# Optimization experiments

Measured on AMD Instinct MI355X. Metric: run time of the kernel, lower is better.

## Reference

```python
import jax, jax.numpy as jnp
import numpy as np

IN_FEATURES = 4096
OUT_FEATURES = 4096
GROUP_SIZE = 128


def _unpack_int4_last_dim(packed):
    # packed: [..., P] int32 -> [..., P*8] int32 nibbles in [0,15]
    shifts = jnp.arange(0, 32, 4, dtype=jnp.int32)
    u = (packed[..., None] >> shifts) & 15
    return u.reshape(*packed.shape[:-1], packed.shape[-1] * 8)


def setup_inputs() -> dict:
    key = jax.random.key(0)
    k1, k2, k3, k4, k5 = jax.random.split(key, 5)
    groups = IN_FEATURES // GROUP_SIZE  # 32
    x = jax.random.normal(k1, (4096, IN_FEATURES), dtype=jnp.float32)
    qweight = jax.random.randint(k2, (OUT_FEATURES, IN_FEATURES // 8), 0, 2147483647, dtype=jnp.int32)
    qzeros = jax.random.randint(k3, (OUT_FEATURES, groups // 8), 0, 2147483647, dtype=jnp.int32)
    scales = jax.random.uniform(k4, (OUT_FEATURES, groups), dtype=jnp.float32) * 0.02 + 0.001
    bias = jax.random.normal(k5, (OUT_FEATURES,), dtype=jnp.float32)
    return {"x": x, "qweight": qweight, "qzeros": qzeros, "scales": scales, "bias": bias}


def _dequantize_weight(qweight, qzeros, scales):
    # qweight: [out, in/8] -> w_int: [out, in]
    w_int = _unpack_int4_last_dim(qweight).astype(jnp.float32)
    # qzeros: [out, groups/8] -> zeros: [out, groups]
    zeros = _unpack_int4_last_dim(qzeros).astype(jnp.float32)
    group_ids = jnp.arange(IN_FEATURES) // GROUP_SIZE  # [in]
    # expand per-group scale/zero along in_features
    w = (w_int - zeros[:, group_ids]) * scales[:, group_ids]  # [out, in]
    return w


def reference(x, qweight, qzeros, scales, bias):
    w = _dequantize_weight(qweight, qzeros, scales)  # [out, in] fp32
    return x @ w.T + bias  # [tokens, out]
```

## Files before the change

### kernel.cpp

```cpp
#include <hip/hip_runtime.h>
#include <hip/hip_bf16.h>

#define TOKENS 4096
#define IN_F   4096
#define OUT_F  4096

typedef __bf16 bf16x8 __attribute__((ext_vector_type(8)));
typedef float  f32x4  __attribute__((ext_vector_type(4)));
typedef unsigned int u32;
typedef u32 u32x4 __attribute__((ext_vector_type(4)));

#define DEQ_BLOCKS 2048
#define CVT_BLOCKS 4096

__device__ __forceinline__ void gld_lds16(const void* g, void* l) {
    __builtin_amdgcn_global_load_lds(
        (const __attribute__((address_space(1))) u32*)g,
        (__attribute__((address_space(3))) u32*)l,
        16, 0, 0);
}

__global__ __launch_bounds__(256) void prep_kernel(
        const u32* __restrict__ qweight, const u32* __restrict__ qzeros,
        const float* __restrict__ scales, const float* __restrict__ x,
        __bf16* __restrict__ W, __bf16* __restrict__ A) {
    const int tid = threadIdx.x;
    if (blockIdx.x < DEQ_BLOCKS) {
        int idx4 = blockIdx.x * 256 + tid;
        int n  = idx4 >> 7;
        int p4 = (idx4 & 127) << 2;
        int g  = p4 >> 4;
        u32 qz = qzeros[(n << 2) + (g >> 3)];
        float z = (float)((qz >> ((g & 7) * 4)) & 15);
        float s = scales[(n << 5) + g];
        u32x4 qw = *(const u32x4*)(qweight + (size_t)n * 512 + p4);
        __bf16* dst = W + (size_t)n * IN_F + p4 * 8;
#pragma unroll
        for (int c = 0; c < 4; ++c) {
            bf16x8 h;
#pragma unroll
            for (int j = 0; j < 8; ++j) {
                float w = ((float)((qw[c] >> (4 * j)) & 15) - z) * s;
                h[j] = (__bf16)w;
            }
            *(bf16x8*)(dst + c * 8) = h;
        }
    } else {
        int idx = (blockIdx.x - DEQ_BLOCKS) * 256 + tid;
        const f32x4* xp = (const f32x4*)x + (size_t)idx * 4;
        f32x4 v0 = xp[0], v1 = xp[1], v2 = xp[2], v3 = xp[3];
        bf16x8 h0, h1;
#pragma unroll
        for (int j = 0; j < 4; ++j) {
            h0[j] = (__bf16)v0[j]; h0[4 + j] = (__bf16)v1[j];
            h1[j] = (__bf16)v2[j]; h1[4 + j] = (__bf16)v3[j];
        }
        bf16x8* ap = (bf16x8*)A + (size_t)idx * 2;
        ap[0] = h0; ap[1] = h1;
    }
}

__global__ __launch_bounds__(512, 2) void gemm8p(
        const __bf16* __restrict__ A, const __bf16* __restrict__ B,
        const float* __restrict__ bias, float* __restrict__ C) {
    __shared__ __align__(16) char lsA[65536];
    __shared__ __align__(16) char lsB[65536];

    const int t    = threadIdx.x;
    const int lane = t & 63, wave = t >> 6;
    const int lr   = lane & 15, quad = lane >> 4;
    const int wm   = (wave >> 2) * 128;
    const int wn   = (wave & 3) * 64;

    int bid = blockIdx.x;
    bid = (bid & 7) * 32 + (bid >> 3);
    const int bm = bid >> 4, bn = bid & 15;

    const __bf16* Abase = A + (size_t)bm * 256 * IN_F;
    const __bf16* Bbase = B + (size_t)bn * 256 * IN_F;

    const int srow0 = t >> 2;
    const int srow1 = 128 + (t >> 2);
    const int scol0 = ((t & 3) ^ ((srow0 >> 1) & 3)) * 8;
    const int scol1 = ((t & 3) ^ ((srow1 >> 1) & 3)) * 8;

#define STAGE(OPBASE, LS, KT, KH, BUF) do {                                  \
    int _kb = (((KT) & 63) * 64 + (KH) * 32);                                \
    gld_lds16(OPBASE + (size_t)srow0 * IN_F + _kb + scol0,                   \
              LS + ((BUF) * 2 + (KH)) * 16384 + t * 16);                     \
    gld_lds16(OPBASE + (size_t)srow1 * IN_F + _kb + scol1,                   \
              LS + ((BUF) * 2 + (KH)) * 16384 + 8192 + t * 16);              \
} while (0)

    const u32 slot16 = (u32)((quad ^ ((lr >> 1) & 3)) * 16);
    const u32 lsA0 = (u32)(size_t)(__attribute__((address_space(3))) char*)lsA;
    const u32 lsB0 = (u32)(size_t)(__attribute__((address_space(3))) char*)lsB;
    const u32 aA = lsA0 + (u32)((wm + lr) * 64) + slot16;
    const u32 aB = lsB0 + (u32)((wn + lr) * 64) + slot16;

    bf16x8 af[4], bfr[4];
    f32x4 acc[8][4] = {};

#define RA(BUF, KH) (((BUF) * 2 + (KH)) * 16384)
#define RB(BUF, KH) (((BUF) * 2 + (KH)) * 16384)

#define DSR(dst, base, OFF) do {                                             \
    u32x4 _r;                                                                \
    asm volatile("ds_read_b128 %0, %1 offset:%2"                             \
                 : "=v"(_r) : "v"(base), "n"(OFF));                          \
    dst = __builtin_bit_cast(bf16x8, _r);                                    \
} while (0)

#define MFMA4_I(PM, I) do {                                                  \
    _Pragma("unroll")                                                        \
    for (int j = 0; j < 4; ++j)                                              \
        acc[(PM) * 4 + (I)][j] = __builtin_amdgcn_mfma_f32_16x16x32_bf16(    \
            af[(I)], bfr[j], acc[(PM) * 4 + (I)][j], 0, 0, 0);               \
} while (0)

#define MFMA4_J(PM, J) do {                                                  \
    _Pragma("unroll")                                                        \
    for (int i = 0; i < 4; ++i)                                              \
        acc[(PM) * 4 + i][(J)] = __builtin_amdgcn_mfma_f32_16x16x32_bf16(    \
            af[i], bfr[(J)], acc[(PM) * 4 + i][(J)], 0, 0, 0);               \
} while (0)

#define FENCE() asm volatile("" ::: "memory")
#define BAR()  do { FENCE(); __builtin_amdgcn_s_barrier(); FENCE(); } while (0)
#define VM6()  asm volatile("s_waitcnt vmcnt(6)" ::: "memory")
#define VM4()  asm volatile("s_waitcnt vmcnt(4)" ::: "memory")
#define PRIO(x) __builtin_amdgcn_s_setprio(x)
#define SB()   __builtin_amdgcn_sched_barrier(0)
#define LGKM0SB() do {                                                       \
    asm volatile("s_waitcnt lgkmcnt(0)" ::: "memory"); SB(); } while (0)

#define P0_BODY(KT, B) do {                                                  \
    STAGE(Abase, lsA, (KT) + 1, 1, 1 - (B));                                 \
    LGKM0SB(); PRIO(1);                                                      \
    MFMA4_I(0,0); SB(); DSR(af[0], aA, RA(B,0)+4096+0*1024); SB();           \
    MFMA4_I(0,1); SB(); DSR(af[1], aA, RA(B,0)+4096+1*1024); SB();           \
    MFMA4_I(0,2); SB(); DSR(af[2], aA, RA(B,0)+4096+2*1024); SB();           \
    MFMA4_I(0,3); SB(); DSR(af[3], aA, RA(B,0)+4096+3*1024); SB();           \
    PRIO(0); BAR();                                                          \
} while (0)

#define P1_BODY(KT, B) do {                                                  \
    STAGE(Bbase, lsB, (KT) + 1, 1, 1 - (B));                                 \
    LGKM0SB(); PRIO(1);                                                      \
    MFMA4_J(1,0); SB(); DSR(bfr[0], aB, RB(B,1)+0*1024); SB();               \
    MFMA4_J(1,1); SB(); DSR(bfr[1], aB, RB(B,1)+1*1024); SB();               \
    MFMA4_J(1,2); SB(); DSR(bfr[2], aB, RB(B,1)+2*1024); SB();               \
    MFMA4_J(1,3); SB(); DSR(bfr[3], aB, RB(B,1)+3*1024); SB();               \
    DSR(af[0], aA, RA(B,1)+0*1024); DSR(af[1], aA, RA(B,1)+1*1024);          \
    DSR(af[2], aA, RA(B,1)+2*1024); DSR(af[3], aA, RA(B,1)+3*1024);          \
    PRIO(0); BAR();                                                          \
} while (0)

#define P2_BODY(KT, B) do {                                                  \
    STAGE(Abase, lsA, (KT) + 2, 0, (B));                                     \
    LGKM0SB(); PRIO(1);                                                      \
    MFMA4_I(0,0); SB(); DSR(af[0], aA, RA(B,1)+4096+0*1024); SB();           \
    MFMA4_I(0,1); SB(); DSR(af[1], aA, RA(B,1)+4096+1*1024); SB();           \
    MFMA4_I(0,2); SB(); DSR(af[2], aA, RA(B,1)+4096+2*1024); SB();           \
    MFMA4_I(0,3); SB(); DSR(af[3], aA, RA(B,1)+4096+3*1024); SB();           \
    PRIO(0); VM6(); BAR();                                                   \
} while (0)

#define P3_BODY(KT, B) do {                                                  \
    STAGE(Bbase, lsB, (KT) + 2, 0, (B));                                     \
    LGKM0SB(); PRIO(1);                                                      \
    MFMA4_J(1,0); SB(); DSR(bfr[0], aB, RB(1-(B),0)+0*1024); SB();           \
    MFMA4_J(1,1); SB(); DSR(bfr[1], aB, RB(1-(B),0)+1*1024); SB();           \
    MFMA4_J(1,2); SB(); DSR(bfr[2], aB, RB(1-(B),0)+2*1024); SB();           \
    MFMA4_J(1,3); SB(); DSR(bfr[3], aB, RB(1-(B),0)+3*1024); SB();           \
    DSR(af[0], aA, RA(1-(B),0)+0*1024); DSR(af[1], aA, RA(1-(B),0)+1*1024);  \
    DSR(af[2], aA, RA(1-(B),0)+2*1024); DSR(af[3], aA, RA(1-(B),0)+3*1024);  \
    PRIO(0); VM4(); BAR();                                                   \
} while (0)

    STAGE(Abase, lsA, 0, 0, 0);
    STAGE(Bbase, lsB, 0, 0, 0);
    STAGE(Abase, lsA, 0, 1, 0);
    STAGE(Bbase, lsB, 0, 1, 0);
    STAGE(Abase, lsA, 1, 0, 1);
    STAGE(Bbase, lsB, 1, 0, 1);
    VM4();
    BAR();
    DSR(bfr[0], aB, RB(0,0)+0*1024); DSR(bfr[1], aB, RB(0,0)+1*1024);
    DSR(bfr[2], aB, RB(0,0)+2*1024); DSR(bfr[3], aB, RB(0,0)+3*1024);
    DSR(af[0], aA, RA(0,0)+0*1024);  DSR(af[1], aA, RA(0,0)+1*1024);
    DSR(af[2], aA, RA(0,0)+2*1024);  DSR(af[3], aA, RA(0,0)+3*1024);

    for (int kt = 0; kt < 64; kt += 2) {
        P0_BODY(kt, 0); P1_BODY(kt, 0); P2_BODY(kt, 0); P3_BODY(kt, 0);
        P0_BODY(kt + 1, 1); P1_BODY(kt + 1, 1);
        P2_BODY(kt + 1, 1); P3_BODY(kt + 1, 1);
    }

    asm volatile("s_waitcnt vmcnt(0) lgkmcnt(0)" ::: "memory");

    const int row0 = bm * 256 + wm + quad * 4;
    const int col0 = bn * 256 + wn + lr;
#pragma unroll
    for (int j = 0; j < 4; ++j) {
        const int col = col0 + j * 16;
        const float bv = bias[col];
#pragma unroll
        for (int i = 0; i < 8; ++i) {
            const int row = row0 + i * 16;
#pragma unroll
            for (int r = 0; r < 4; ++r)
                C[(size_t)(row + r) * OUT_F + col] = acc[i][j][r] + bv;
        }
    }
}

extern "C" void kernel_launch(void* const* d_in, const int* in_sizes, int n_in,
                              void* d_out, int out_size, void* d_ws, size_t ws_size,
                              hipStream_t stream) {
    (void)in_sizes; (void)n_in; (void)out_size; (void)ws_size;
    const float* x       = (const float*)d_in[0];
    const u32*   qweight = (const u32*)d_in[1];
    const u32*   qzeros  = (const u32*)d_in[2];
    const float* scales  = (const float*)d_in[3];
    const float* bias    = (const float*)d_in[4];
    float* out = (float*)d_out;

    __bf16* W   = (__bf16*)d_ws;
    __bf16* Abf = (__bf16*)((char*)d_ws + (size_t)OUT_F * IN_F * 2);

    prep_kernel<<<dim3(DEQ_BLOCKS + CVT_BLOCKS), dim3(256), 0, stream>>>(
        qweight, qzeros, scales, x, W, Abf);
    gemm8p<<<dim3(256), dim3(512), 0, stream>>>(Abf, W, bias, out);
}
```

Measured before the change: 240.2 us.

## Double-buffer A/B fragment registers to overlap LDS reads with MFMA phases

```diff
diff --git a/kernel.cpp b/kernel.cpp
--- a/kernel.cpp
+++ b/kernel.cpp
@@ -98,7 +98,7 @@
     const u32 aA = lsA0 + (u32)((wm + lr) * 64) + slot16;
     const u32 aB = lsB0 + (u32)((wn + lr) * 64) + slot16;
 
-    bf16x8 af[4], bfr[4];
+    bf16x8 af0[4], af1[4], bf0[4], bf1[4];
     f32x4 acc[8][4] = {};
 
 #define RA(BUF, KH) (((BUF) * 2 + (KH)) * 16384)
@@ -111,18 +111,11 @@
     dst = __builtin_bit_cast(bf16x8, _r);                                    \
 } while (0)
 
-#define MFMA4_I(PM, I) do {                                                  \
+#define G4(PM, I, AF, BF) do {                                               \
     _Pragma("unroll")                                                        \
     for (int j = 0; j < 4; ++j)                                              \
         acc[(PM) * 4 + (I)][j] = __builtin_amdgcn_mfma_f32_16x16x32_bf16(    \
-            af[(I)], bfr[j], acc[(PM) * 4 + (I)][j], 0, 0, 0);               \
-} while (0)
-
-#define MFMA4_J(PM, J) do {                                                  \
-    _Pragma("unroll")                                                        \
-    for (int i = 0; i < 4; ++i)                                              \
-        acc[(PM) * 4 + i][(J)] = __builtin_amdgcn_mfma_f32_16x16x32_bf16(    \
-            af[i], bfr[(J)], acc[(PM) * 4 + i][(J)], 0, 0, 0);               \
+            AF[(I)], BF[j], acc[(PM) * 4 + (I)][j], 0, 0, 0);                \
 } while (0)
 
 #define FENCE() asm volatile("" ::: "memory")
@@ -137,45 +130,49 @@
 #define P0_BODY(KT, B) do {                                                  \
     STAGE(Abase, lsA, (KT) + 1, 1, 1 - (B));                                 \
     LGKM0SB(); PRIO(1);                                                      \
-    MFMA4_I(0,0); SB(); DSR(af[0], aA, RA(B,0)+4096+0*1024); SB();           \
-    MFMA4_I(0,1); SB(); DSR(af[1], aA, RA(B,0)+4096+1*1024); SB();           \
-    MFMA4_I(0,2); SB(); DSR(af[2], aA, RA(B,0)+4096+2*1024); SB();           \
-    MFMA4_I(0,3); SB(); DSR(af[3], aA, RA(B,0)+4096+3*1024); SB();           \
+    G4(0,0,af0,bf0); SB(); DSR(af1[0], aA, RA(B,0)+4096+0*1024);             \
+                           DSR(bf1[0], aB, RB(B,1)+0*1024); SB();            \
+    G4(0,1,af0,bf0); SB(); DSR(af1[1], aA, RA(B,0)+4096+1*1024);             \
+                           DSR(bf1[1], aB, RB(B,1)+1*1024); SB();            \
+    G4(0,2,af0,bf0); SB(); DSR(af1[2], aA, RA(B,0)+4096+2*1024);             \
+                           DSR(bf1[2], aB, RB(B,1)+2*1024); SB();            \
+    G4(0,3,af0,bf0); SB(); DSR(af1[3], aA, RA(B,0)+4096+3*1024);             \
+                           DSR(bf1[3], aB, RB(B,1)+3*1024); SB();            \
     PRIO(0); BAR();                                                          \
 } while (0)
 
 #define P1_BODY(KT, B) do {                                                  \
     STAGE(Bbase, lsB, (KT) + 1, 1, 1 - (B));                                 \
     LGKM0SB(); PRIO(1);                                                      \
-    MFMA4_J(1,0); SB(); DSR(bfr[0], aB, RB(B,1)+0*1024); SB();               \
-    MFMA4_J(1,1); SB(); DSR(bfr[1], aB, RB(B,1)+1*1024); SB();               \
-    MFMA4_J(1,2); SB(); DSR(bfr[2], aB, RB(B,1)+2*1024); SB();               \
-    MFMA4_J(1,3); SB(); DSR(bfr[3], aB, RB(B,1)+3*1024); SB();               \
-    DSR(af[0], aA, RA(B,1)+0*1024); DSR(af[1], aA, RA(B,1)+1*1024);          \
-    DSR(af[2], aA, RA(B,1)+2*1024); DSR(af[3], aA, RA(B,1)+3*1024);          \
+    G4(1,0,af1,bf0); SB(); DSR(af0[0], aA, RA(B,1)+0*1024); SB();            \
+    G4(1,1,af1,bf0); SB(); DSR(af0[1], aA, RA(B,1)+1*1024); SB();            \
+    G4(1,2,af1,bf0); SB(); DSR(af0[2], aA, RA(B,1)+2*1024); SB();            \
+    G4(1,3,af1,bf0); SB(); DSR(af0[3], aA, RA(B,1)+3*1024); SB();            \
     PRIO(0); BAR();                                                          \
 } while (0)
 
 #define P2_BODY(KT, B) do {                                                  \
     STAGE(Abase, lsA, (KT) + 2, 0, (B));                                     \
-    LGKM0SB(); PRIO(1);                                                      \
-    MFMA4_I(0,0); SB(); DSR(af[0], aA, RA(B,1)+4096+0*1024); SB();           \
-    MFMA4_I(0,1); SB(); DSR(af[1], aA, RA(B,1)+4096+1*1024); SB();           \
-    MFMA4_I(0,2); SB(); DSR(af[2], aA, RA(B,1)+4096+2*1024); SB();           \
-    MFMA4_I(0,3); SB(); DSR(af[3], aA, RA(B,1)+4096+3*1024); SB();           \
-    PRIO(0); VM6(); BAR();                                                   \
+    VM6(); LGKM0SB(); PRIO(1);                                               \
+    G4(0,0,af0,bf1); SB(); DSR(af1[0], aA, RA(B,1)+4096+0*1024);             \
+                           DSR(bf0[0], aB, RB(1-(B),0)+0*1024); SB();        \
+    G4(0,1,af0,bf1); SB(); DSR(af1[1], aA, RA(B,1)+4096+1*1024);             \
+                           DSR(bf0[1], aB, RB(1-(B),0)+1*1024); SB();        \
+    G4(0,2,af0,bf1); SB(); DSR(af1[2], aA, RA(B,1)+4096+2*1024);             \
+                           DSR(bf0[2], aB, RB(1-(B),0)+2*1024); SB();        \
+    G4(0,3,af0,bf1); SB(); DSR(af1[3], aA, RA(B,1)+4096+3*1024);             \
+                           DSR(bf0[3], aB, RB(1-(B),0)+3*1024); SB();        \
+    PRIO(0); BAR();                                                          \
 } while (0)
 
 #define P3_BODY(KT, B) do {                                                  \
     STAGE(Bbase, lsB, (KT) + 2, 0, (B));                                     \
-    LGKM0SB(); PRIO(1);                                                      \
-    MFMA4_J(1,0); SB(); DSR(bfr[0], aB, RB(1-(B),0)+0*1024); SB();           \
-    MFMA4_J(1,1); SB(); DSR(bfr[1], aB, RB(1-(B),0)+1*1024); SB();           \
-    MFMA4_J(1,2); SB(); DSR(bfr[2], aB, RB(1-(B),0)+2*1024); SB();           \
-    MFMA4_J(1,3); SB(); DSR(bfr[3], aB, RB(1-(B),0)+3*1024); SB();           \
-    DSR(af[0], aA, RA(1-(B),0)+0*1024); DSR(af[1], aA, RA(1-(B),0)+1*1024);  \
-    DSR(af[2], aA, RA(1-(B),0)+2*1024); DSR(af[3], aA, RA(1-(B),0)+3*1024);  \
-    PRIO(0); VM4(); BAR();                                                   \
+    VM4(); LGKM0SB(); PRIO(1);                                               \
+    G4(1,0,af1,bf1); SB(); DSR(af0[0], aA, RA(1-(B),0)+0*1024); SB();        \
+    G4(1,1,af1,bf1); SB(); DSR(af0[1], aA, RA(1-(B),0)+1*1024); SB();        \
+    G4(1,2,af1,bf1); SB(); DSR(af0[2], aA, RA(1-(B),0)+2*1024); SB();        \
+    G4(1,3,af1,bf1); SB(); DSR(af0[3], aA, RA(1-(B),0)+3*1024); SB();        \
+    PRIO(0); BAR();                                                          \
 } while (0)
 
     STAGE(Abase, lsA, 0, 0, 0);
@@ -186,10 +183,10 @@
     STAGE(Bbase, lsB, 1, 0, 1);
     VM4();
     BAR();
-    DSR(bfr[0], aB, RB(0,0)+0*1024); DSR(bfr[1], aB, RB(0,0)+1*1024);
-    DSR(bfr[2], aB, RB(0,0)+2*1024); DSR(bfr[3], aB, RB(0,0)+3*1024);
-    DSR(af[0], aA, RA(0,0)+0*1024);  DSR(af[1], aA, RA(0,0)+1*1024);
-    DSR(af[2], aA, RA(0,0)+2*1024);  DSR(af[3], aA, RA(0,0)+3*1024);
+    DSR(bf0[0], aB, RB(0,0)+0*1024); DSR(bf0[1], aB, RB(0,0)+1*1024);
+    DSR(bf0[2], aB, RB(0,0)+2*1024); DSR(bf0[3], aB, RB(0,0)+3*1024);
+    DSR(af0[0], aA, RA(0,0)+0*1024); DSR(af0[1], aA, RA(0,0)+1*1024);
+    DSR(af0[2], aA, RA(0,0)+2*1024); DSR(af0[3], aA, RA(0,0)+3*1024);
 
     for (int kt = 0; kt < 64; kt += 2) {
         P0_BODY(kt, 0); P1_BODY(kt, 0); P2_BODY(kt, 0); P3_BODY(kt, 0);
```

New measurement: 246.4 us. +2.6%, slower.
